# Kernel tuning notes

Measured on AMD Instinct MI355X. Metric: run time of the kernel, lower is better.

Reference implementation:

```python
import jax, jax.numpy as jnp
import numpy as np


def setup_inputs() -> dict:
    key = jax.random.key(0)
    k1, k2, k3 = jax.random.split(key, 3)
    B, D, T = 16, 64, 8192
    n_codebook, n_emb = 4, 512
    z_e_x = jax.random.normal(k1, (B, D, T), dtype=jnp.float32)
    # torch init is uniform(-1/n_emb, 1/n_emb)
    codebook = jax.random.uniform(k2, (n_codebook, D, n_emb), dtype=jnp.float32,
                                  minval=-1.0 / n_emb, maxval=1.0 / n_emb)
    codebook_index = jax.random.randint(k3, (1,), 0, n_codebook, dtype=jnp.int64)
    return {"z_e_x": z_e_x, "codebook": codebook, "codebook_index": codebook_index}


def reference(z_e_x, codebook, codebook_index):
    # codebook: [n_codebook, D, n_emb]; select one codebook -> [D, n_emb]
    cb = codebook[codebook_index[0]]
    B, D, T = z_e_x.shape
    # [B, D, T] -> [B*T, D]
    z = jnp.transpose(z_e_x, (0, 2, 1)).reshape(-1, D)
    # squared L2 distances to each code: [B*T, n_emb]
    dist2 = (jnp.sum(z * z, axis=1, keepdims=True)
             - 2.0 * (z @ cb)
             + jnp.sum(cb * cb, axis=0))
    z_id_flat = jnp.argmax(-dist2, axis=1)          # nearest code index, [B*T]
    z_id = z_id_flat.reshape(B, T)
    z_q = cb.T[z_id_flat].reshape(B, T, D)          # gather codes
    z_q = jnp.transpose(z_q, (0, 2, 1))             # [B, D, T]
    return z_q, z_id
```

## Files before the change

### kernel.cpp

```cpp
#include <hip/hip_runtime.h>


constexpr int Dc = 64, Ec = 512, Tc = 8192;
constexpr int QTOT = 131072, ZQ = 8388608;

using short8 = __attribute__((ext_vector_type(8))) short;
using f32x16 = __attribute__((ext_vector_type(16))) float;

__device__ __forceinline__ unsigned short bf16rn(float f) {
    unsigned u = __float_as_uint(f);
    unsigned r = u + 0x7FFFu + ((u >> 16) & 1u);
    return (unsigned short)(r >> 16);
}

__global__ void vq_prep(const float* __restrict__ cbfull, const int* __restrict__ cbidx,
                        unsigned short* __restrict__ ws16) {
    int tid = blockIdx.x * 256 + threadIdx.x;
    if (tid >= 16 * 4 * 64) return;
    int l = tid & 63, c = (tid >> 6) & 3, g = tid >> 8;
    const float* cb = cbfull + (size_t)(cbidx[0] & 3) * (Dc * Ec);
    int n = g * 32 + (l & 31);
    int kbase = c * 16 + (l >> 5) * 8;
    size_t bh = ((size_t)((g * 4 + c) * 2 + 0) * 512) + l * 8;
    size_t bl = ((size_t)((g * 4 + c) * 2 + 1) * 512) + l * 8;
    #pragma unroll
    for (int i = 0; i < 8; ++i) {
        float v = cb[(kbase + i) * Ec + n];
        unsigned short h = bf16rn(v);
        float hf = __uint_as_float((unsigned)h << 16);
        ws16[bh + i] = h;
        ws16[bl + i] = bf16rn(v - hf);
    }
}

__global__ __launch_bounds__(256) void vq_main(
    const float* __restrict__ z, const float* __restrict__ cbfull,
    const int* __restrict__ cbidx, const unsigned short* __restrict__ ws16,
    float* __restrict__ out) {
    __shared__ unsigned s_B[8192];
    __shared__ float s_c2[Ec];
    __shared__ unsigned s_w[128];
    __shared__ int s_idx[128];

    const int tid = threadIdx.x;
    const int lane = tid & 63;
    const int wave = __builtin_amdgcn_readfirstlane(tid >> 6);
    const int q0 = blockIdx.x * 128;
    const int b = q0 >> 13;
    const int t0 = q0 & (Tc - 1);
    const int col = lane & 31;
    const int hh = lane >> 5;
    const int myq = wave * 32 + col;
    const int t = t0 + myq;

    const int ci = cbidx[0] & 3;
    const float* __restrict__ cb = cbfull + (size_t)ci * (Dc * Ec);

    float zv[32];
    const float* zp = z + (size_t)b * Dc * Tc + t;
    #pragma unroll
    for (int c = 0; c < 4; ++c)
        #pragma unroll
        for (int i = 0; i < 8; ++i)
            zv[c * 8 + i] = zp[(size_t)(c * 16 + hh * 8 + i) * Tc];

    for (int j = tid; j < Ec; j += 256) {
        float cc = cb[j];
        float a = __fmul_rn(cc, cc);
        for (int d = 1; d < Dc; ++d) { cc = cb[d * Ec + j]; a = __fadd_rn(a, __fmul_rn(cc, cc)); }
        s_c2[j] = a;
    }

    float s1p = 0.f;
    #pragma unroll
    for (int e = 0; e < 32; ++e) s1p = __fmaf_rn(zv[e], zv[e], s1p);
    float s1b = (s1p + __shfl_xor(s1p, 32, 64)) * 1.001f + 0.01f;
    float wf = 3.1e-7f * (s1b + 1.f) + 4.2e-6f * sqrtf(s1b) + 2.1e-5f;
    unsigned w_int = (s1b > 880.f) ? 0x7FFFFFFFu : (unsigned)(wf * 2.147483648e9f) + 512u;
    if (lane < 32) s_w[myq] = w_int;

    short8 uhf[4], ulf[4];
    #pragma unroll
    for (int c = 0; c < 4; ++c)
        #pragma unroll
        for (int i = 0; i < 8; ++i) {
            float f = -2.0f * zv[c * 8 + i];
            unsigned short h = bf16rn(f);
            float hf = __uint_as_float((unsigned)h << 16);
            uhf[c][i] = (short)h;
            ulf[c][i] = (short)bf16rn(f - hf);
        }

    unsigned m1[16], m2[16];
    #pragma unroll
    for (int r = 0; r < 16; ++r) { m1[r] = 0xFFFFFFFFu; m2[r] = 0xFFFFFFFFu; }

    for (int chk = 0; chk < 4; ++chk) {
        __syncthreads();
        #pragma unroll
        for (int s = 0; s < 8; ++s) {
            int lslot = wave * 8 + s;
            int gs = lslot >> 3, cc = (lslot >> 1) & 3, hl = lslot & 1;
            int gslot = ((chk * 4 + gs) * 4 + cc) * 2 + hl;
            const uint4 v = *(const uint4*)(ws16 + (size_t)gslot * 512 + lane * 8);
            *(uint4*)((char*)s_B + lslot * 1024 + lane * 16) = v;
        }
        __syncthreads();

        for (int gs = 0; gs < 4; ++gs) {
            int g = chk * 4 + gs;
            short8 chf[4], clf[4];
            #pragma unroll
            for (int c = 0; c < 4; ++c) {
                chf[c] = *(const short8*)((const char*)s_B + (((gs * 4 + c) * 2 + 0) * 1024) + lane * 16);
                clf[c] = *(const short8*)((const char*)s_B + (((gs * 4 + c) * 2 + 1) * 1024) + lane * 16);
            }
            float kb = s_c2[g * 32 + col];
            f32x16 acc;
            #pragma unroll
            for (int r = 0; r < 16; ++r) acc[r] = kb;
            #pragma unroll
            for (int c = 0; c < 4; ++c) {
                acc = __builtin_amdgcn_mfma_f32_32x32x16_bf16(uhf[c], chf[c], acc, 0, 0, 0);
                acc = __builtin_amdgcn_mfma_f32_32x32x16_bf16(uhf[c], clf[c], acc, 0, 0, 0);
                acc = __builtin_amdgcn_mfma_f32_32x32x16_bf16(ulf[c], chf[c], acc, 0, 0, 0);
            }
            unsigned jj = (unsigned)(g * 32 + col);
            #pragma unroll
            for (int r = 0; r < 16; ++r) {
                unsigned key = (__float_as_uint(acc[r] + 3.0f) << 9) | jj;
                unsigned mx = key > m1[r] ? key : m1[r];
                m1[r] = key < m1[r] ? key : m1[r];
                m2[r] = mx < m2[r] ? mx : m2[r];
            }
        }
    }
    __syncthreads();

    #pragma unroll
    for (int r = 0; r < 16; ++r) {
        int row = (r & 3) + 8 * (r >> 2) + 4 * hh;
        unsigned* p = s_B + (((wave * 32 + row) * 32) + col) * 2;
        p[0] = m1[r]; p[1] = m2[r];
    }
    __syncthreads();

    int qq = lane >> 1, hf = lane & 1;
    const unsigned* p = s_B + (((wave * 32 + qq) * 32) + hf * 16) * 2;
    unsigned M1 = 0xFFFFFFFFu, M2 = 0xFFFFFFFFu;
    #pragma unroll
    for (int e = 0; e < 32; ++e) {
        unsigned v = p[e];
        unsigned mx = v > M1 ? v : M1;
        M1 = v < M1 ? v : M1;
        M2 = mx < M2 ? mx : M2;
    }
    {
        unsigned o1 = __shfl_xor(M1, 1, 64);
        unsigned o2 = __shfl_xor(M2, 1, 64);
        unsigned mx = M1 > o1 ? M1 : o1;
        M1 = M1 < o1 ? M1 : o1;
        M2 = M2 < o2 ? M2 : o2;
        M2 = mx < M2 ? mx : M2;
    }
    if ((lane & 1) == 0) s_idx[wave * 32 + qq] = (int)(M1 & 511u);
    unsigned wq = s_w[wave * 32 + qq];
    bool resc = ((unsigned long long)M2 <= (unsigned long long)M1 + wq);
    unsigned long long mask = __ballot(resc && ((lane & 1) == 0));

    while (mask) {
        int L = __ffsll((unsigned long long)mask) - 1; mask &= mask - 1;
        int ql = L >> 1;
        const float* zq = z + (size_t)b * Dc * Tc + (t0 + wave * 32 + ql);
        float zr[64];
        #pragma unroll
        for (int d = 0; d < 64; ++d) zr[d] = zq[(size_t)d * Tc];
        float rr[8];
        #pragma unroll
        for (int u = 0; u < 8; ++u) rr[u] = __fmul_rn(zr[u], zr[u]);
        #pragma unroll
        for (int i = 8; i < 64; i += 8)
            #pragma unroll
            for (int u = 0; u < 8; ++u)
                rr[u] = __fadd_rn(rr[u], __fmul_rn(zr[i + u], zr[i + u]));
        float s1 = __fadd_rn(__fadd_rn(__fadd_rn(rr[0], rr[1]), __fadd_rn(rr[2], rr[3])),
                             __fadd_rn(__fadd_rn(rr[4], rr[5]), __fadd_rn(rr[6], rr[7])));
        float bk = __int_as_float(0x7f800000);
        int bj = 0;
        for (int u = 0; u < 8; ++u) {
            int j = u * 64 + lane;
            float G = 0.f;
            #pragma unroll
            for (int d = 0; d < 64; ++d) G = __fmaf_rn(zr[d], cb[d * Ec + j], G);
            float key = __fadd_rn(__fsub_rn(s1, __fmul_rn(2.0f, G)), s_c2[j]);
            if (key < bk) { bk = key; bj = j; }
        }
        #pragma unroll
        for (int m = 1; m < 64; m <<= 1) {
            float pk = __shfl_xor(bk, m, 64);
            int pj = __shfl_xor(bj, m, 64);
            if (pk < bk || (pk == bk && pj < bj)) { bk = pk; bj = pj; }
        }
        if (lane == 0) s_idx[wave * 32 + ql] = bj;
    }
    __syncthreads();

    for (int qh = 0; qh < 2; ++qh) {
        int ql = qh * 64 + lane;
        int jj = s_idx[ql];
        int tt = t0 + ql;
        #pragma unroll
        for (int dd = 0; dd < 16; ++dd) {
            int d = wave * 16 + dd;
            out[((size_t)b * Dc + d) * Tc + tt] = cb[d * Ec + jj];
        }
        if (wave == 0) out[ZQ + q0 + ql] = (float)jj;
    }
}

extern "C" void kernel_launch(void* const* d_in, const int* in_sizes, int n_in,
                              void* d_out, int out_size, void* d_ws, size_t ws_size,
                              hipStream_t stream) {
    const float* z = (const float*)d_in[0];
    const float* cbfull = (const float*)d_in[1];
    const int* cbidx = (const int*)d_in[2];
    unsigned short* ws16 = (unsigned short*)d_ws;
    float* out = (float*)d_out;

    hipLaunchKernelGGL(vq_prep, dim3(16), dim3(256), 0, stream, cbfull, cbidx, ws16);
    hipLaunchKernelGGL(vq_main, dim3(QTOT / 128), dim3(256), 0, stream,
                       z, cbfull, cbidx, ws16, out);
}
```

Baseline: 96.98 us.

## Split codebook across wave pairs, drop LDS staging, precompute code norms

Each block now handles 64 queries instead of 128, and the two waves sharing a query tile each scan half of the codebook. The two halves' top-2 results are merged through small shared arrays. The bf16 codebook fragments are read straight from global memory (L2-cached) instead of being staged through a 32KB LDS buffer with per-chunk barriers. Code squared norms move into the prep kernel rather than being recomputed in every block. This cuts shared memory and barriers so more blocks can be resident (launch bounds 5), at the cost of twice as many blocks, more global fragment loads, and a shuffle-based top-2 reduction.

```diff
diff --git a/kernel.cpp b/kernel.cpp
--- a/kernel.cpp
+++ b/kernel.cpp
@@ -3,6 +3,7 @@
 
 constexpr int Dc = 64, Ec = 512, Tc = 8192;
 constexpr int QTOT = 131072, ZQ = 8388608;
+constexpr int QPB = 64;
 
 using short8 = __attribute__((ext_vector_type(8))) short;
 using f32x16 = __attribute__((ext_vector_type(16))) float;
@@ -16,9 +17,16 @@
 __global__ void vq_prep(const float* __restrict__ cbfull, const int* __restrict__ cbidx,
                         unsigned short* __restrict__ ws16) {
     int tid = blockIdx.x * 256 + threadIdx.x;
+    const float* cb = cbfull + (size_t)(cbidx[0] & 3) * (Dc * Ec);
+    if (tid < 512) {
+        int j = tid;
+        float c = cb[j];
+        float a = __fmul_rn(c, c);
+        for (int d = 1; d < Dc; ++d) { c = cb[d * Ec + j]; a = __fadd_rn(a, __fmul_rn(c, c)); }
+        ((float*)(ws16 + 65536))[j] = a;
+    }
     if (tid >= 16 * 4 * 64) return;
     int l = tid & 63, c = (tid >> 6) & 3, g = tid >> 8;
-    const float* cb = cbfull + (size_t)(cbidx[0] & 3) * (Dc * Ec);
     int n = g * 32 + (l & 31);
     int kbase = c * 16 + (l >> 5) * 8;
     size_t bh = ((size_t)((g * 4 + c) * 2 + 0) * 512) + l * 8;
@@ -33,29 +41,30 @@
     }
 }
 
-__global__ __launch_bounds__(256) void vq_main(
+__global__ __launch_bounds__(256, 5) void vq_main(
     const float* __restrict__ z, const float* __restrict__ cbfull,
     const int* __restrict__ cbidx, const unsigned short* __restrict__ ws16,
     float* __restrict__ out) {
-    __shared__ unsigned s_B[8192];
     __shared__ float s_c2[Ec];
-    __shared__ unsigned s_w[128];
-    __shared__ int s_idx[128];
+    __shared__ unsigned s_w[QPB];
+    __shared__ int s_idx[QPB];
+    __shared__ unsigned s_p1[QPB], s_p2[QPB];
 
     const int tid = threadIdx.x;
     const int lane = tid & 63;
     const int wave = __builtin_amdgcn_readfirstlane(tid >> 6);
-    const int q0 = blockIdx.x * 128;
-    const int b = q0 >> 13;
-    const int t0 = q0 & (Tc - 1);
-    const int col = lane & 31;
-    const int hh = lane >> 5;
-    const int myq = wave * 32 + col;
+    const int qt = wave >> 1, half = wave & 1;
+    const int col = lane & 31, hh = lane >> 5;
+    const int q0 = blockIdx.x * QPB;
+    const int b = q0 >> 13, t0 = q0 & (Tc - 1);
+    const int myq = qt * 32 + col;
     const int t = t0 + myq;
 
     const int ci = cbidx[0] & 3;
     const float* __restrict__ cb = cbfull + (size_t)ci * (Dc * Ec);
 
+    for (int j = tid; j < Ec; j += 256) s_c2[j] = ((const float*)(ws16 + 65536))[j];
+
     float zv[32];
     const float* zp = z + (size_t)b * Dc * Tc + t;
     #pragma unroll
@@ -63,13 +72,6 @@
         #pragma unroll
         for (int i = 0; i < 8; ++i)
             zv[c * 8 + i] = zp[(size_t)(c * 16 + hh * 8 + i) * Tc];
-
-    for (int j = tid; j < Ec; j += 256) {
-        float cc = cb[j];
-        float a = __fmul_rn(cc, cc);
-        for (int d = 1; d < Dc; ++d) { cc = cb[d * Ec + j]; a = __fadd_rn(a, __fmul_rn(cc, cc)); }
-        s_c2[j] = a;
-    }
 
     float s1p = 0.f;
     #pragma unroll
@@ -77,7 +79,7 @@
     float s1b = (s1p + __shfl_xor(s1p, 32, 64)) * 1.001f + 0.01f;
     float wf = 3.1e-7f * (s1b + 1.f) + 4.2e-6f * sqrtf(s1b) + 2.1e-5f;
     unsigned w_int = (s1b > 880.f) ? 0x7FFFFFFFu : (unsigned)(wf * 2.147483648e9f) + 512u;
-    if (lane < 32) s_w[myq] = w_int;
+    if (half == 0 && lane < 32) s_w[myq] = w_int;
 
     short8 uhf[4], ulf[4];
     #pragma unroll
@@ -91,87 +93,85 @@
             ulf[c][i] = (short)bf16rn(f - hf);
         }
 
+    __syncthreads();
+
     unsigned m1[16], m2[16];
     #pragma unroll
     for (int r = 0; r < 16; ++r) { m1[r] = 0xFFFFFFFFu; m2[r] = 0xFFFFFFFFu; }
 
-    for (int chk = 0; chk < 4; ++chk) {
-        __syncthreads();
-        #pragma unroll
-        for (int s = 0; s < 8; ++s) {
-            int lslot = wave * 8 + s;
-            int gs = lslot >> 3, cc = (lslot >> 1) & 3, hl = lslot & 1;
-            int gslot = ((chk * 4 + gs) * 4 + cc) * 2 + hl;
-            const uint4 v = *(const uint4*)(ws16 + (size_t)gslot * 512 + lane * 8);
-            *(uint4*)((char*)s_B + lslot * 1024 + lane * 16) = v;
-        }
-        __syncthreads();
-
-        for (int gs = 0; gs < 4; ++gs) {
-            int g = chk * 4 + gs;
-            short8 chf[4], clf[4];
-            #pragma unroll
-            for (int c = 0; c < 4; ++c) {
-                chf[c] = *(const short8*)((const char*)s_B + (((gs * 4 + c) * 2 + 0) * 1024) + lane * 16);
-                clf[c] = *(const short8*)((const char*)s_B + (((gs * 4 + c) * 2 + 1) * 1024) + lane * 16);
-            }
-            float kb = s_c2[g * 32 + col];
-            f32x16 acc;
-            #pragma unroll
-            for (int r = 0; r < 16; ++r) acc[r] = kb;
-            #pragma unroll
-            for (int c = 0; c < 4; ++c) {
-                acc = __builtin_amdgcn_mfma_f32_32x32x16_bf16(uhf[c], chf[c], acc, 0, 0, 0);
-                acc = __builtin_amdgcn_mfma_f32_32x32x16_bf16(uhf[c], clf[c], acc, 0, 0, 0);
-                acc = __builtin_amdgcn_mfma_f32_32x32x16_bf16(ulf[c], chf[c], acc, 0, 0, 0);
-            }
-            unsigned jj = (unsigned)(g * 32 + col);
-            #pragma unroll
-            for (int r = 0; r < 16; ++r) {
-                unsigned key = (__float_as_uint(acc[r] + 3.0f) << 9) | jj;
-                unsigned mx = key > m1[r] ? key : m1[r];
-                m1[r] = key < m1[r] ? key : m1[r];
-                m2[r] = mx < m2[r] ? mx : m2[r];
-            }
+    #pragma unroll 2
+    for (int gi = 0; gi < 8; ++gi) {
+        const int g = half * 8 + gi;
+        const unsigned short* fb = ws16 + (size_t)(g * 8) * 512;
+        const float kb = s_c2[g * 32 + col];
+        f32x16 acc;
+        #pragma unroll
+        for (int r = 0; r < 16; ++r) acc[r] = kb;
+        #pragma unroll
+        for (int c = 0; c < 4; ++c) {
+            short8 chf = *(const short8*)(fb + (size_t)(c * 2 + 0) * 512 + lane * 8);
+            short8 clf = *(const short8*)(fb + (size_t)(c * 2 + 1) * 512 + lane * 8);
+            acc = __builtin_amdgcn_mfma_f32_32x32x16_bf16(uhf[c], chf, acc, 0, 0, 0);
+            acc = __builtin_amdgcn_mfma_f32_32x32x16_bf16(uhf[c], clf, acc, 0, 0, 0);
+            acc = __builtin_amdgcn_mfma_f32_32x32x16_bf16(ulf[c], chf, acc, 0, 0, 0);
+        }
+        const unsigned jj = (unsigned)(g * 32 + col);
+        #pragma unroll
+        for (int r = 0; r < 16; ++r) {
+            unsigned key = (__float_as_uint(acc[r] + 3.0f) << 9) | jj;
+            unsigned mx = key > m1[r] ? key : m1[r];
+            m1[r] = key < m1[r] ? key : m1[r];
+            m2[r] = mx < m2[r] ? mx : m2[r];
+        }
+    }
+
+    #pragma unroll
+    for (int st = 1; st < 32; st <<= 1) {
+        #pragma unroll
+        for (int r = 0; r < 16; ++r) {
+            unsigned o1 = __shfl_xor(m1[r], st, 64);
+            unsigned o2 = __shfl_xor(m2[r], st, 64);
+            unsigned mx = m1[r] > o1 ? m1[r] : o1;
+            m1[r] = m1[r] < o1 ? m1[r] : o1;
+            m2[r] = m2[r] < o2 ? m2[r] : o2;
+            m2[r] = m2[r] < mx ? m2[r] : mx;
+        }
+    }
+
+    #pragma unroll
+    for (int r = 0; r < 16; ++r) {
+        if (half == 0 && col == r) {
+            int row = (r & 3) + 8 * (r >> 2) + 4 * hh;
+            s_p1[qt * 32 + row] = m1[r];
+            s_p2[qt * 32 + row] = m2[r];
         }
     }
     __syncthreads();
 
+    unsigned long long mask = 0;
     #pragma unroll
     for (int r = 0; r < 16; ++r) {
-        int row = (r & 3) + 8 * (r >> 2) + 4 * hh;
-        unsigned* p = s_B + (((wave * 32 + row) * 32) + col) * 2;
-        p[0] = m1[r]; p[1] = m2[r];
-    }
-    __syncthreads();
-
-    int qq = lane >> 1, hf = lane & 1;
-    const unsigned* p = s_B + (((wave * 32 + qq) * 32) + hf * 16) * 2;
-    unsigned M1 = 0xFFFFFFFFu, M2 = 0xFFFFFFFFu;
-    #pragma unroll
-    for (int e = 0; e < 32; ++e) {
-        unsigned v = p[e];
-        unsigned mx = v > M1 ? v : M1;
-        M1 = v < M1 ? v : M1;
-        M2 = mx < M2 ? mx : M2;
-    }
-    {
-        unsigned o1 = __shfl_xor(M1, 1, 64);
-        unsigned o2 = __shfl_xor(M2, 1, 64);
-        unsigned mx = M1 > o1 ? M1 : o1;
-        M1 = M1 < o1 ? M1 : o1;
-        M2 = M2 < o2 ? M2 : o2;
-        M2 = mx < M2 ? mx : M2;
-    }
-    if ((lane & 1) == 0) s_idx[wave * 32 + qq] = (int)(M1 & 511u);
-    unsigned wq = s_w[wave * 32 + qq];
-    bool resc = ((unsigned long long)M2 <= (unsigned long long)M1 + wq);
-    unsigned long long mask = __ballot(resc && ((lane & 1) == 0));
+        bool amb = false;
+        if (half == 1 && col == r) {
+            int row = (r & 3) + 8 * (r >> 2) + 4 * hh;
+            int Q = qt * 32 + row;
+            unsigned a1 = s_p1[Q], a2 = s_p2[Q];
+            unsigned mx = a1 > m1[r] ? a1 : m1[r];
+            unsigned F1 = a1 < m1[r] ? a1 : m1[r];
+            unsigned F2 = a2 < m2[r] ? a2 : m2[r];
+            F2 = F2 < mx ? F2 : mx;
+            s_idx[Q] = (int)(F1 & 511u);
+            unsigned wq = s_w[Q];
+            amb = ((unsigned long long)F2 <= (unsigned long long)F1 + wq);
+        }
+        mask |= __ballot(amb);
+    }
 
     while (mask) {
-        int L = __ffsll((unsigned long long)mask) - 1; mask &= mask - 1;
-        int ql = L >> 1;
-        const float* zq = z + (size_t)b * Dc * Tc + (t0 + wave * 32 + ql);
+        int L = __ffsll(mask) - 1; mask &= mask - 1;
+        int r = L & 31, hb = L >> 5;
+        int Q = qt * 32 + (r & 3) + 8 * (r >> 2) + 4 * hb;
+        const float* zq = z + (size_t)b * Dc * Tc + (t0 + Q);
         float zr[64];
         #pragma unroll
         for (int d = 0; d < 64; ++d) zr[d] = zq[(size_t)d * Tc];
@@ -201,20 +201,18 @@
             int pj = __shfl_xor(bj, m, 64);
             if (pk < bk || (pk == bk && pj < bj)) { bk = pk; bj = pj; }
         }
-        if (lane == 0) s_idx[wave * 32 + ql] = bj;
+        if (lane == 0) s_idx[Q] = bj;
     }
     __syncthreads();
 
-    for (int qh = 0; qh < 2; ++qh) {
-        int ql = qh * 64 + lane;
-        int jj = s_idx[ql];
-        int tt = t0 + ql;
-        #pragma unroll
-        for (int dd = 0; dd < 16; ++dd) {
-            int d = wave * 16 + dd;
-            out[((size_t)b * Dc + d) * Tc + tt] = cb[d * Ec + jj];
-        }
-        if (wave == 0) out[ZQ + q0 + ql] = (float)jj;
+    {
+        const int jj = s_idx[lane];
+        const int tt = t0 + lane;
+        float* op = out + ((size_t)b * Dc + wave * 16) * Tc + tt;
+        #pragma unroll
+        for (int dd = 0; dd < 16; ++dd)
+            op[(size_t)dd * Tc] = cb[(wave * 16 + dd) * Ec + jj];
+        if (wave == 0) out[ZQ + q0 + lane] = (float)jj;
     }
 }
 
@@ -228,6 +226,6 @@
     float* out = (float*)d_out;
 
     hipLaunchKernelGGL(vq_prep, dim3(16), dim3(256), 0, stream, cbfull, cbidx, ws16);
-    hipLaunchKernelGGL(vq_main, dim3(QTOT / 128), dim3(256), 0, stream,
+    hipLaunchKernelGGL(vq_main, dim3(QTOT / QPB), dim3(256), 0, stream,
                        z, cbfull, cbidx, ws16, out);
 }
```

New measurement: 282.6 us. +191.4%, slower.
